# Optimization experiments

Hardware: AMD Instinct MI355X
Metric: run time of the kernel (lower is better)

The kernel has to match this reference:

```python
import jax, jax.numpy as jnp
import numpy as np

B, S, LW = 64, 128, 20
CHAR_V, CHAR_E, CHAR_C = 100, 30, 30
WORD_V, WORD_E = 100000, 300
H, NC = 256, 25
F = WORD_E + CHAR_C  # 330


def setup_inputs() -> dict:
    key = jax.random.key(0)
    ks = jax.random.split(key, 16)
    u = lambda k, shape, s: jax.random.uniform(k, shape, jnp.float32, -s, s)
    sent = jax.random.randint(ks[0], (B, S), 0, WORD_V)
    word = jax.random.randint(ks[1], (B, S, LW), 0, CHAR_V)
    tag = jax.random.randint(ks[2], (B, S), 0, NC)
    lengths = jax.random.randint(ks[3], (B,), S // 2, S + 1)
    mask = jnp.arange(S)[None, :] < lengths[:, None]  # [B,S] bool, mask[:,0] all True

    word_table = u(ks[4], (WORD_V, WORD_E), 0.5)
    char_table = u(ks[5], (CHAR_V, CHAR_E), (3.0 / CHAR_E) ** 0.5)
    conv_w = u(ks[6], (CHAR_C, CHAR_E, 3), (6.0 / (CHAR_E * 3 + CHAR_C)) ** 0.5)
    conv_b = jnp.zeros((CHAR_C,), jnp.float32)

    def lstm_params(k):
        k1, k2 = jax.random.split(k)
        s_ih = (6.0 / (4 * H + F)) ** 0.5
        s_hh = (6.0 / (4 * H + H)) ** 0.5
        w_ih = u(k1, (4 * H, F), s_ih)
        w_hh = u(k2, (4 * H, H), s_hh)
        # b_ih + b_hh, each with forget-gate slice [H:2H] = 1.0 -> combined 2.0
        b = jnp.zeros((4 * H,), jnp.float32).at[H:2 * H].set(2.0)
        return w_ih, w_hh, b

    w_ih_f, w_hh_f, b_f = lstm_params(ks[7])
    w_ih_r, w_hh_r, b_r = lstm_params(ks[8])
    s_lin = (6.0 / (NC + 2 * H)) ** 0.5
    lin_w = u(ks[9], (NC, 2 * H), s_lin)
    lin_b = jnp.zeros((NC,), jnp.float32)
    start_t = u(ks[10], (NC,), 0.1)
    end_t = u(ks[11], (NC,), 0.1)
    trans = u(ks[12], (NC, NC), 0.1)
    return dict(word_table=word_table, char_table=char_table, conv_w=conv_w,
                conv_b=conv_b, w_ih_f=w_ih_f, w_hh_f=w_hh_f, b_f=b_f,
                w_ih_r=w_ih_r, w_hh_r=w_hh_r, b_r=b_r, lin_w=lin_w, lin_b=lin_b,
                start_t=start_t, end_t=end_t, trans=trans,
                sent=sent, word=word, tag=tag, mask=mask)


def _lstm_dir(x, w_ih, w_hh, b, reverse):
    # x: [B,S,F] -> precompute input projections time-major [S,B,4H]
    gx = jnp.einsum('bsf,gf->sbg', x, w_ih) + b
    bsz = x.shape[0]
    hs = w_hh.shape[1]

    def step(carry, g):
        h, c = carry
        g = g + h @ w_hh.T
        i, f, gg, o = jnp.split(g, 4, axis=-1)
        c = jax.nn.sigmoid(f) * c + jax.nn.sigmoid(i) * jnp.tanh(gg)
        h = jax.nn.sigmoid(o) * jnp.tanh(c)
        return (h, c), h

    init = (jnp.zeros((bsz, hs), x.dtype), jnp.zeros((bsz, hs), x.dtype))
    _, hseq = jax.lax.scan(step, init, gx, reverse=reverse)
    return hseq  # [S,B,H]


def _crf_nll(em, tg, mk, start_t, end_t, trans):
    # em: [S,B,C] emissions; tg: [S,B] int; mk: [S,B] float (mk[0]=1)
    bsz = em.shape[1]
    bidx = jnp.arange(bsz)
    # numerator: gold path score
    em_tag = jnp.take_along_axis(em, tg[..., None], axis=-1)[..., 0]   # [S,B]
    tr = trans[tg[:-1], tg[1:]]                                        # [S-1,B]
    score = start_t[tg[0]] + em_tag[0] + jnp.sum(mk[1:] * (tr + em_tag[1:]), axis=0)
    last = mk.sum(0).astype(jnp.int32) - 1
    score = score + end_t[tg[last, bidx]]
    # denominator: forward algorithm (logsumexp scan over time)
    alpha0 = start_t[None, :] + em[0]                                   # [B,C]

    def step(alpha, xs):
        em_t, mk_t = xs
        nxt = jax.nn.logsumexp(alpha[:, :, None] + trans[None, :, :] + em_t[:, None, :], axis=1)
        alpha = jnp.where(mk_t[:, None] > 0, nxt, alpha)
        return alpha, None

    alpha, _ = jax.lax.scan(step, alpha0, (em[1:], mk[1:]))
    logZ = jax.nn.logsumexp(alpha + end_t[None, :], axis=1)
    return -jnp.sum(score - logZ)  # model returns -log_likelihood (reduction='sum')


def reference(word_table, char_table, conv_w, conv_b, w_ih_f, w_hh_f, b_f,
              w_ih_r, w_hh_r, b_r, lin_w, lin_b, start_t, end_t, trans,
              sent, word, tag, mask):
    # --- char CNN encoder (dropout = identity in eval; no ReLU in original forward) ---
    ct = char_table.at[0].set(0.0)                      # padding_idx=0
    cemb = ct[word]                                     # [B,S,LW,E]
    x = cemb.reshape(B * S, LW, CHAR_E).transpose(0, 2, 1)  # [BS,E,LW]
    conv = jax.lax.conv_general_dilated(
        x, conv_w, window_strides=(1,), padding=[(1, 1)],
        dimension_numbers=('NCH', 'OIH', 'NCH')) + conv_b[None, :, None]
    char_feat = conv.max(axis=2).reshape(B, S, CHAR_C)  # global max-pool over chars
    # --- word embedding + concat ---
    wemb = word_table[sent]                             # [B,S,WORD_E]
    feat = jnp.concatenate([wemb, char_feat], axis=2)   # [B,S,F]
    # --- biLSTM ---
    hf = _lstm_dir(feat, w_ih_f, w_hh_f, b_f, reverse=False)
    hr = _lstm_dir(feat, w_ih_r, w_hh_r, b_r, reverse=True)
    h = jnp.concatenate([hf, hr], axis=-1)              # [S,B,2H] time-major
    em = h @ lin_w.T + lin_b                            # [S,B,NC]
    # --- CRF negative log-likelihood ---
    tg = tag.T
    mk = mask.T.astype(em.dtype)
    return _crf_nll(em, tg, mk, start_t, end_t, trans)
```

## Files before the change

### kernel.cpp

```cpp
#include <hip/hip_runtime.h>
#include <math.h>

#define B_  64
#define S_  128
#define LW_ 20
#define CHAR_E_ 30
#define CHAR_C_ 30
#define WORD_E_ 300
#define H_  256
#define NC_ 25
#define F_  330
#define KP_ 352
#define G4_ 1024
#define NG_ 2048

typedef __attribute__((ext_vector_type(8))) short short8;
typedef __attribute__((ext_vector_type(4))) float floatx4;
typedef __attribute__((ext_vector_type(8))) int int8v;

__device__ __forceinline__ float sigmoidf_(float x){ return 1.0f/(1.0f+__expf(-x)); }
__device__ __forceinline__ float tanh_(float x){ return 1.0f - 2.0f/(1.0f+__expf(2.0f*x)); }

__device__ __forceinline__ unsigned int f2bf(float f){
    unsigned int u = __float_as_uint(f);
    u += 0x7FFFu + ((u>>16)&1u);
    return (u>>16) & 0xFFFFu;
}
__device__ __forceinline__ float bf2f(unsigned int v){ return __uint_as_float(v<<16); }

__device__ __forceinline__ void gload16(const void* g, void* l){
    __builtin_amdgcn_global_load_lds((const __attribute__((address_space(1))) unsigned int*)g,
                                     (__attribute__((address_space(3))) unsigned int*)l, 16, 0, 0);
}

#define BAR_LDS() __asm__ volatile("s_waitcnt lgkmcnt(0)\n\ts_barrier" ::: "memory")

__global__ __launch_bounds__(256) void k_prep(const float* ct, const int* word,
        const float* cw, const float* cb, const float* wt, const int* sent,
        const float* wf, const float* wr, float* out,
        unsigned short* feat, unsigned short* wpack){
    __shared__ __align__(16) float x[8][32][20];
    int blk = blockIdx.x;
    int tid = threadIdx.x;
    if(blk < 1024){
        int tok0 = blk*8;
        for(int e = tid; e < 8*32*20; e += 256){
            int t  = e % 20;
            int ic = (e/20) & 31;
            int tl = e / 640;
            int id = word[(size_t)(tok0+tl)*LW_ + t];
            float v = 0.f;
            if(ic < CHAR_E_ && id != 0) v = ct[(size_t)id*CHAR_E_ + ic];
            x[tl][ic][t] = v;
        }
        __syncthreads();
        if(tid < 240){
            int tl = tid/30, oc = tid%30;
            float acc[22];
            #pragma unroll
            for(int q=0;q<22;q++) acc[q] = 0.f;
            for(int ic=0; ic<CHAR_E_; ic++){
                float w0 = cw[(oc*CHAR_E_+ic)*3+0];
                float w1 = cw[(oc*CHAR_E_+ic)*3+1];
                float w2 = cw[(oc*CHAR_E_+ic)*3+2];
                const float* xr = &x[tl][ic][0];
                #pragma unroll
                for(int t4=0;t4<5;t4++){
                    float4 v = ((const float4*)xr)[t4];
                    int t0 = t4*4;
                    acc[t0+2] += v.x*w0; acc[t0+1] += v.x*w1; acc[t0+0] += v.x*w2;
                    acc[t0+3] += v.y*w0; acc[t0+2] += v.y*w1; acc[t0+1] += v.y*w2;
                    acc[t0+4] += v.z*w0; acc[t0+3] += v.z*w1; acc[t0+2] += v.z*w2;
                    acc[t0+5] += v.w*w0; acc[t0+4] += v.w*w1; acc[t0+3] += v.w*w2;
                }
            }
            float m = -1e30f;
            #pragma unroll
            for(int t=0;t<20;t++){ float v = acc[t+1]; m = fmaxf(m, v); }
            m += cb[oc];
            feat[(size_t)(tok0+tl)*KP_ + WORD_E_ + oc] = (unsigned short)f2bf(m);
        }
    } else if(blk < 1024+2432){
        int idx = (blk-1024)*256 + tid;
        int n = idx / 76, e4 = idx % 76;
        if(e4 < 75){
            float4 v = ((const float4*)(wt + (size_t)sent[n]*WORD_E_))[e4];
            unsigned int lo = f2bf(v.x) | (f2bf(v.y)<<16);
            unsigned int hi = f2bf(v.z) | (f2bf(v.w)<<16);
            uint2 pr; pr.x = lo; pr.y = hi;
            *(uint2*)(feat + (size_t)n*KP_ + e4*4) = pr;
        } else {
            unsigned int* z = (unsigned int*)(feat + (size_t)n*KP_ + 330);
            #pragma unroll
            for(int q=0;q<11;q++) z[q] = 0;
        }
    } else if(blk < 6272){
        int i = (blk-3456)*256 + tid;
        int r = i / KP_, k = i % KP_;
        const float* src = (r < G4_) ? wf : wr;
        int rr = r & (G4_-1);
        wpack[i] = (k < F_) ? (unsigned short)f2bf(src[(size_t)rr*F_ + k]) : 0;
    } else {
        if(tid == 0) *out = 0.f;
    }
}

__global__ __launch_bounds__(256) void k_gemm(const unsigned short* A, const unsigned short* Bw,
                                              const float* bf, const float* br, unsigned short* gxb){
    __shared__ __align__(16) unsigned short As[128*32];
    __shared__ __align__(16) unsigned short Bs[128*32];
    int m0 = blockIdx.x*128, n0 = blockIdx.y*128;
    int tid = threadIdx.x;
    int w = tid>>6, lane = tid&63, q = lane>>4, l16 = lane&15;
    int wr = w>>1, wc = w&1;
    int srow0 = w*32 + (lane>>2);
    int scol  = (lane&3)*8;
    floatx4 acc[4][4];
    #pragma unroll
    for(int i=0;i<4;i++)
        #pragma unroll
        for(int j=0;j<4;j++) acc[i][j] = (floatx4){0.f,0.f,0.f,0.f};

    for(int k0=0; k0<KP_; k0+=32){
        __syncthreads();
        gload16(A  + (size_t)(m0+srow0   )*KP_ + k0 + scol, (unsigned short*)As + w*1024      );
        gload16(A  + (size_t)(m0+srow0+16)*KP_ + k0 + scol, (unsigned short*)As + w*1024 + 512);
        gload16(Bw + (size_t)(n0+srow0   )*KP_ + k0 + scol, (unsigned short*)Bs + w*1024      );
        gload16(Bw + (size_t)(n0+srow0+16)*KP_ + k0 + scol, (unsigned short*)Bs + w*1024 + 512);
        __asm__ volatile("s_waitcnt vmcnt(0)" ::: "memory");
        __syncthreads();
        short8 a_[4], b_[4];
        #pragma unroll
        for(int i=0;i<4;i++) a_[i] = *(const short8*)&As[(wr*64 + i*16 + l16)*32 + q*8];
        #pragma unroll
        for(int j=0;j<4;j++) b_[j] = *(const short8*)&Bs[(wc*64 + j*16 + l16)*32 + q*8];
        #pragma unroll
        for(int i=0;i<4;i++)
            #pragma unroll
            for(int j=0;j<4;j++)
                acc[i][j] = __builtin_amdgcn_mfma_f32_16x16x32_bf16(a_[i], b_[j], acc[i][j], 0,0,0);
    }
    #pragma unroll
    for(int j=0;j<4;j++){
        int n = n0 + wc*64 + j*16 + l16;
        int dirr = n >> 10, grow = n & 1023;
        float bias = dirr ? br[grow] : bf[grow];
        #pragma unroll
        for(int i=0;i<4;i++){
            int mb = m0 + wr*64 + i*16 + q*4;
            #pragma unroll
            for(int r=0;r<4;r++){
                gxb[(size_t)(mb+r)*NG_ + n] = (unsigned short)f2bf(acc[i][j][r] + bias);
            }
        }
    }
}

__device__ __forceinline__ void lstm_step(
    const unsigned char* hbb, unsigned char* hwr_slot,
    float* wreg_lds, const int8v (*wreg)[2][2],
    int l16, int q, int cbl, int urel,
    unsigned int G0, unsigned int G1, unsigned int G2, unsigned int G3,
    float& cc, float* hseq_ptr, const float inv_sc)
{
    floatx4 a00={0.f,0.f,0.f,0.f}, a01=a00, a10=a00, a11=a00,
            a20=a00, a21=a00, a30=a00, a31=a00;
    #pragma unroll
    for(int ki=0; ki<2; ki++){
        int8v hb = *(const int8v*)&hbb[l16*272 + ki*128 + q*32];
        a00 = __builtin_amdgcn_mfma_scale_f32_16x16x128_f8f6f4(wreg[0][0][ki], hb, a00, 0,0,0,0x7F,0,0x7F);
        a01 = __builtin_amdgcn_mfma_scale_f32_16x16x128_f8f6f4(wreg[0][1][ki], hb, a01, 0,0,0,0x7F,0,0x7F);
        a10 = __builtin_amdgcn_mfma_scale_f32_16x16x128_f8f6f4(wreg[1][0][ki], hb, a10, 0,0,0,0x7F,0,0x7F);
        a11 = __builtin_amdgcn_mfma_scale_f32_16x16x128_f8f6f4(wreg[1][1][ki], hb, a11, 0,0,0,0x7F,0,0x7F);
        a20 = __builtin_amdgcn_mfma_scale_f32_16x16x128_f8f6f4(wreg[2][0][ki], hb, a20, 0,0,0,0x7F,0,0x7F);
        a21 = __builtin_amdgcn_mfma_scale_f32_16x16x128_f8f6f4(wreg[2][1][ki], hb, a21, 0,0,0,0x7F,0,0x7F);
        a30 = __builtin_amdgcn_mfma_scale_f32_16x16x128_f8f6f4(wreg[3][0][ki], hb, a30, 0,0,0,0x7F,0,0x7F);
        a31 = __builtin_amdgcn_mfma_scale_f32_16x16x128_f8f6f4(wreg[3][1][ki], hb, a31, 0,0,0,0x7F,0,0x7F);
    }
    if(l16 < 2){
        int base = l16*32 + q*4;
        *(floatx4*)&wreg_lds[0*64 + base     ] = a00;
        *(floatx4*)&wreg_lds[0*64 + base + 16] = a01;
        *(floatx4*)&wreg_lds[1*64 + base     ] = a10;
        *(floatx4*)&wreg_lds[1*64 + base + 16] = a11;
        *(floatx4*)&wreg_lds[2*64 + base     ] = a20;
        *(floatx4*)&wreg_lds[2*64 + base + 16] = a21;
        *(floatx4*)&wreg_lds[3*64 + base     ] = a30;
        *(floatx4*)&wreg_lds[3*64 + base + 16] = a31;
    }
    int cidx = cbl*32 + urel;
    float iv = wreg_lds[0*64 + cidx]*inv_sc + bf2f(G0);
    float fv = wreg_lds[1*64 + cidx]*inv_sc + bf2f(G1);
    float gv = wreg_lds[2*64 + cidx]*inv_sc + bf2f(G2);
    float ov = wreg_lds[3*64 + cidx]*inv_sc + bf2f(G3);
    float cn = sigmoidf_(fv)*cc + sigmoidf_(iv)*tanh_(gv);
    cc = cn;
    float hv = sigmoidf_(ov)*tanh_(cn);
    *hseq_ptr = hv;
    unsigned int hp8 = __builtin_amdgcn_cvt_pk_fp8_f32(hv*16.f, hv*16.f, 0u, false);
    *hwr_slot = (unsigned char)(hp8 & 0xFF);
    BAR_LDS();
}

__global__ __launch_bounds__(512,2) void k_lstm_all(const float* whhf, const float* whhr,
        const unsigned short* gxb, float* hseq)
{
    int bid = blockIdx.x;
    int dir = bid >> 5;
    int bg  = bid & 31;
    int tid = threadIdx.x;
    int w    = tid >> 6;
    int lane = tid & 63;
    int q    = lane >> 4;
    int l16  = lane & 15;

    __shared__ __align__(16) unsigned char hlds[2][16*272];
    __shared__ __align__(16) float wregion[8*256];

    const float* whh = dir ? whhr : whhf;

    int8v wreg[4][2][2];
    #pragma unroll
    for(int g=0; g<4; g++){
        #pragma unroll
        for(int j=0; j<2; j++){
            const float* rp = whh + (size_t)(g*H_ + w*32 + j*16 + l16)*H_;
            #pragma unroll
            for(int ki=0; ki<2; ki++){
                const float* p = rp + ki*128 + q*32;
                int8v acc;
                #pragma unroll
                for(int wd=0; wd<8; wd++){
                    unsigned int d = 0;
                    d = __builtin_amdgcn_cvt_pk_fp8_f32(p[wd*4+0]*64.f, p[wd*4+1]*64.f, d, false);
                    d = __builtin_amdgcn_cvt_pk_fp8_f32(p[wd*4+2]*64.f, p[wd*4+3]*64.f, d, true);
                    acc[wd] = (int)d;
                }
                wreg[g][j][ki] = acc;
            }
        }
    }

    for(int i = tid; i < 2*16*272/4; i += 512) ((unsigned int*)hlds)[i] = 0;
    __syncthreads();

    int urel = lane & 31;
    int cbl  = lane >> 5;
    int cu   = w*32 + urel;
    int b_glob = bg*2 + cbl;
    const float inv_sc = 1.0f/1024.f;

    float cc = 0.f;
    const unsigned short* gbase = gxb + (size_t)b_glob*S_*NG_ + (size_t)dir*G4_ + cu;
    float* hseq_base = hseq + ((size_t)dir*S_*B_ + b_glob)*H_ + cu;
    unsigned char* hw0 = &hlds[0][cbl*272 + cu];
    unsigned char* hw1 = &hlds[1][cbl*272 + cu];
    float* wreg_lds = &wregion[w*256];

    unsigned int p0,p1,p2,p3, q0,q1,q2,q3;
    {
        const unsigned short* gp = gbase + (size_t)(dir ? (S_-1) : 0)*NG_;
        p0 = gp[0]; p1 = gp[256]; p2 = gp[512]; p3 = gp[768];
    }

    for(int t=0; t<S_; t+=2){
        int sA = dir ? (S_-1-t) : t;
        int sB = dir ? (S_-2-t) : (t+1);
        int sC = (t+2 < S_) ? (dir ? (S_-3-t) : (t+2)) : sB;

        {
            const unsigned short* gp = gbase + (size_t)sB*NG_;
            q0 = gp[0]; q1 = gp[256]; q2 = gp[512]; q3 = gp[768];
        }
        lstm_step(&hlds[0][0], hw1, wreg_lds, wreg, l16, q, cbl, urel,
                  p0,p1,p2,p3, cc, hseq_base + (size_t)sA*B_*H_, inv_sc);

        {
            const unsigned short* gp = gbase + (size_t)sC*NG_;
            p0 = gp[0]; p1 = gp[256]; p2 = gp[512]; p3 = gp[768];
        }
        lstm_step(&hlds[1][0], hw0, wreg_lds, wreg, l16, q, cbl, urel,
                  q0,q1,q2,q3, cc, hseq_base + (size_t)sB*B_*H_, inv_sc);
    }
}

__global__ __launch_bounds__(256) void k_em(const float* hseq, const float* lw, const float* lb, float* em){
    __shared__ __align__(16) float hb[8][516];
    int sb0 = blockIdx.x*8;
    int tid = threadIdx.x;
    for(int i = tid; i < 1024; i += 256){
        int p = i >> 7, r = i & 127;
        int sb = sb0 + p, s = sb >> 6, b = sb & 63;
        const float* src = (r < 64) ? (hseq + (((size_t)0*S_+s)*B_+b)*H_ + r*4)
                                    : (hseq + (((size_t)1*S_+s)*B_+b)*H_ + (r-64)*4);
        *(float4*)&hb[p][r*4] = *(const float4*)src;
    }
    __syncthreads();
    if(tid < 200){
        int p = tid / 25, nc = tid % 25;
        const float4* wv = (const float4*)(lw + (size_t)nc*2*H_);
        const float4* hv = (const float4*)&hb[p][0];
        float acc = lb[nc];
        #pragma unroll 16
        for(int k=0;k<128;k++){ float4 a=hv[k], ww=wv[k]; acc += a.x*ww.x + a.y*ww.y + a.z*ww.z + a.w*ww.w; }
        em[(size_t)(sb0+p)*NC_ + nc] = acc;
    }
}

__global__ void k_crf(const float* em, const int* tag, const void* mask,
                      const float* st, const float* et, const float* tr, float* out){
    __shared__ float trs[NC_*NC_];
    int b = blockIdx.x, tid = threadIdx.x;
    for(int i=tid;i<NC_*NC_;i+=64) trs[i]=tr[i];
    unsigned int first = *(const unsigned int*)mask;
    int ml;
    if(first == 1u) ml = 0;
    else if(first == 0x3F800000u) ml = 2;
    else ml = 1;
    __syncthreads();

    float part = 0.f; int cnt = 0;
    for(int s = tid; s < S_; s += 64){
        float mkv;
        {
            int off = b*S_ + s;
            if(ml==0)      mkv = ((const int*)mask)[off] ? 1.f : 0.f;
            else if(ml==1) mkv = ((const unsigned char*)mask)[off] ? 1.f : 0.f;
            else           mkv = ((const float*)mask)[off];
        }
        cnt += (mkv != 0.f) ? 1 : 0;
        if(s == 0){
            int t0 = tag[b*S_];
            part += st[t0] + em[((size_t)0*B_ + b)*NC_ + t0];
        } else {
            int tp = tag[b*S_ + s-1], tc = tag[b*S_ + s];
            part += mkv * (trs[tp*NC_ + tc] + em[((size_t)s*B_ + b)*NC_ + tc]);
        }
    }
    for(int o=32;o>0;o>>=1){ part += __shfl_down(part, o); cnt += __shfl_down(cnt, o); }
    float score = 0.f;
    int len = __shfl(cnt, 0);
    float score0 = __shfl(part, 0);
    if(tid == 0) score = score0 + et[ tag[b*S_ + len-1] ];

    float Ecol[NC_];
    if(tid < NC_){
        #pragma unroll
        for(int i=0;i<NC_;i++) Ecol[i] = __expf(trs[i*NC_+tid]);
    } else {
        #pragma unroll
        for(int i=0;i<NC_;i++) Ecol[i] = 0.f;
    }

    float alpha = (tid < NC_) ? (st[tid] + em[((size_t)0*B_ + b)*NC_ + tid]) : -1e30f;
    float em_n = (tid < NC_) ? em[((size_t)1*B_ + b)*NC_ + tid] : 0.f;

    for(int s=1;s<S_;s++){
        float em_c = em_n;
        if(s+1 < S_) em_n = (tid < NC_) ? em[((size_t)(s+1)*B_ + b)*NC_ + tid] : 0.f;
        float mkv;
        {
            int off = b*S_ + s;
            if(ml==0)      mkv = ((const int*)mask)[off] ? 1.f : 0.f;
            else if(ml==1) mkv = ((const unsigned char*)mask)[off] ? 1.f : 0.f;
            else           mkv = ((const float*)mask)[off];
        }
        float v = alpha;
        #pragma unroll
        for(int o=16;o>0;o>>=1) v = fmaxf(v, __shfl_down(v, o));
        float m = __shfl(v, 0);
        float a = (tid < NC_) ? __expf(alpha - m) : 0.f;
        float S0 = 0.f, S1 = 0.f;
        #pragma unroll
        for(int i=0;i<24;i+=2){ S0 += __shfl(a, i) * Ecol[i]; S1 += __shfl(a, i+1) * Ecol[i+1]; }
        S0 += __shfl(a, 24) * Ecol[24];
        float nxt = m + __logf(S0 + S1) + em_c;
        if(tid < NC_ && mkv != 0.f) alpha = nxt;
    }

    float v = (tid < NC_) ? (alpha + et[tid]) : -1e30f;
    float m2 = v;
    #pragma unroll
    for(int o=16;o>0;o>>=1) m2 = fmaxf(m2, __shfl_down(m2, o));
    m2 = __shfl(m2, 0);
    float e = (tid < NC_) ? __expf(v - m2) : 0.f;
    #pragma unroll
    for(int o=16;o>0;o>>=1) e += __shfl_down(e, o);
    if(tid == 0){
        float logZ = m2 + __logf(e);
        atomicAdd(out, logZ - score);
    }
}

extern "C" void kernel_launch(void* const* d_in, const int* in_sizes, int n_in,
                              void* d_out, int out_size, void* d_ws, size_t ws_size,
                              hipStream_t stream) {
    const float* word_table = (const float*)d_in[0];
    const float* char_table = (const float*)d_in[1];
    const float* conv_w     = (const float*)d_in[2];
    const float* conv_b     = (const float*)d_in[3];
    const float* w_ih_f     = (const float*)d_in[4];
    const float* w_hh_f     = (const float*)d_in[5];
    const float* b_f        = (const float*)d_in[6];
    const float* w_ih_r     = (const float*)d_in[7];
    const float* w_hh_r     = (const float*)d_in[8];
    const float* b_r        = (const float*)d_in[9];
    const float* lin_w      = (const float*)d_in[10];
    const float* lin_b      = (const float*)d_in[11];
    const float* start_t    = (const float*)d_in[12];
    const float* end_t      = (const float*)d_in[13];
    const float* trans      = (const float*)d_in[14];
    const int*   sent       = (const int*)d_in[15];
    const int*   word       = (const int*)d_in[16];
    const int*   tag        = (const int*)d_in[17];
    const void*  mask       = d_in[18];
    float* out = (float*)d_out;

    char* ws = (char*)d_ws;
    unsigned short* feat  = (unsigned short*)ws;
    unsigned short* wpack = (unsigned short*)(ws + 5767168);
    unsigned short* gxb   = (unsigned short*)(ws + 5767168 + 1441792);
    float* hseq = (float*)(ws + 5767168 + 1441792 + 33554432);
    float* em   = (float*)(ws + 5767168 + 1441792 + 33554432 + 16777216);

    k_prep<<<dim3(6273), 256, 0, stream>>>(char_table, word, conv_w, conv_b,
                                           word_table, sent, w_ih_f, w_ih_r, out, feat, wpack);
    k_gemm<<<dim3(B_*S_/128, NG_/128), 256, 0, stream>>>(feat, wpack, b_f, b_r, gxb);
    k_lstm_all<<<dim3(64), 512, 0, stream>>>(w_hh_f, w_hh_r, gxb, hseq);
    k_em<<<dim3(S_*B_/8), 256, 0, stream>>>(hseq, lin_w, lin_b, em);
    k_crf<<<dim3(B_), 64, 0, stream>>>(em, tag, mask, start_t, end_t, trans, out);
}
```

Before: 569.2 us.

## Process 16 batch rows per LSTM block using full MFMA output, drop LDS gate exchange

The recurrent LSTM kernel previously used 64 blocks, each handling 2 batch rows, so most of each 16-wide MFMA output was wasted. The gates then went through an LDS round-trip so each thread could pick one unit. Now each block handles 16 batch rows, and each lane applies the cell update directly on its own accumulator registers (8 values per lane). It also writes h and the fp8 copy as vectors and prefetches packed bf16 gate inputs. The grid drops from 64 to 8 blocks. That removes the redundant MFMA work and one LDS exchange plus reads per step, but leaves most CUs idle and puts more elementwise work on each thread.

```diff
diff --git a/kernel.cpp b/kernel.cpp
--- a/kernel.cpp
+++ b/kernel.cpp
@@ -27,6 +27,11 @@
     return (u>>16) & 0xFFFFu;
 }
 __device__ __forceinline__ float bf2f(unsigned int v){ return __uint_as_float(v<<16); }
+
+__device__ __forceinline__ float bfh(uint2 pk, int r){
+    unsigned int w = (r < 2) ? pk.x : pk.y;
+    return __uint_as_float((r & 1) ? (w & 0xffff0000u) : (w << 16));
+}
 
 __device__ __forceinline__ void gload16(const void* g, void* l){
     __builtin_amdgcn_global_load_lds((const __attribute__((address_space(1))) unsigned int*)g,
@@ -156,49 +161,47 @@
     }
 }
 
-__device__ __forceinline__ void lstm_step(
-    const unsigned char* hbb, unsigned char* hwr_slot,
-    float* wreg_lds, const int8v (*wreg)[2][2],
-    int l16, int q, int cbl, int urel,
-    unsigned int G0, unsigned int G1, unsigned int G2, unsigned int G3,
-    float& cc, float* hseq_ptr, const float inv_sc)
+__device__ __forceinline__ void lstm_step16(
+    const unsigned char* hbb, unsigned char* hpub,
+    const int8v (*wreg)[2][2],
+    int l16, int q,
+    const uint2 (&gg)[4][2],
+    float (&cc)[2][4], float* hs_ptr, const float inv_sc)
 {
-    floatx4 a00={0.f,0.f,0.f,0.f}, a01=a00, a10=a00, a11=a00,
-            a20=a00, a21=a00, a30=a00, a31=a00;
+    floatx4 a[4][2];
+    #pragma unroll
+    for(int g=0; g<4; g++){
+        a[g][0] = (floatx4){0.f,0.f,0.f,0.f};
+        a[g][1] = (floatx4){0.f,0.f,0.f,0.f};
+    }
     #pragma unroll
     for(int ki=0; ki<2; ki++){
         int8v hb = *(const int8v*)&hbb[l16*272 + ki*128 + q*32];
-        a00 = __builtin_amdgcn_mfma_scale_f32_16x16x128_f8f6f4(wreg[0][0][ki], hb, a00, 0,0,0,0x7F,0,0x7F);
-        a01 = __builtin_amdgcn_mfma_scale_f32_16x16x128_f8f6f4(wreg[0][1][ki], hb, a01, 0,0,0,0x7F,0,0x7F);
-        a10 = __builtin_amdgcn_mfma_scale_f32_16x16x128_f8f6f4(wreg[1][0][ki], hb, a10, 0,0,0,0x7F,0,0x7F);
-        a11 = __builtin_amdgcn_mfma_scale_f32_16x16x128_f8f6f4(wreg[1][1][ki], hb, a11, 0,0,0,0x7F,0,0x7F);
-        a20 = __builtin_amdgcn_mfma_scale_f32_16x16x128_f8f6f4(wreg[2][0][ki], hb, a20, 0,0,0,0x7F,0,0x7F);
-        a21 = __builtin_amdgcn_mfma_scale_f32_16x16x128_f8f6f4(wreg[2][1][ki], hb, a21, 0,0,0,0x7F,0,0x7F);
-        a30 = __builtin_amdgcn_mfma_scale_f32_16x16x128_f8f6f4(wreg[3][0][ki], hb, a30, 0,0,0,0x7F,0,0x7F);
-        a31 = __builtin_amdgcn_mfma_scale_f32_16x16x128_f8f6f4(wreg[3][1][ki], hb, a31, 0,0,0,0x7F,0,0x7F);
-    }
-    if(l16 < 2){
-        int base = l16*32 + q*4;
-        *(floatx4*)&wreg_lds[0*64 + base     ] = a00;
-        *(floatx4*)&wreg_lds[0*64 + base + 16] = a01;
-        *(floatx4*)&wreg_lds[1*64 + base     ] = a10;
-        *(floatx4*)&wreg_lds[1*64 + base + 16] = a11;
-        *(floatx4*)&wreg_lds[2*64 + base     ] = a20;
-        *(floatx4*)&wreg_lds[2*64 + base + 16] = a21;
-        *(floatx4*)&wreg_lds[3*64 + base     ] = a30;
-        *(floatx4*)&wreg_lds[3*64 + base + 16] = a31;
-    }
-    int cidx = cbl*32 + urel;
-    float iv = wreg_lds[0*64 + cidx]*inv_sc + bf2f(G0);
-    float fv = wreg_lds[1*64 + cidx]*inv_sc + bf2f(G1);
-    float gv = wreg_lds[2*64 + cidx]*inv_sc + bf2f(G2);
-    float ov = wreg_lds[3*64 + cidx]*inv_sc + bf2f(G3);
-    float cn = sigmoidf_(fv)*cc + sigmoidf_(iv)*tanh_(gv);
-    cc = cn;
-    float hv = sigmoidf_(ov)*tanh_(cn);
-    *hseq_ptr = hv;
-    unsigned int hp8 = __builtin_amdgcn_cvt_pk_fp8_f32(hv*16.f, hv*16.f, 0u, false);
-    *hwr_slot = (unsigned char)(hp8 & 0xFF);
+        #pragma unroll
+        for(int g=0; g<4; g++){
+            a[g][0] = __builtin_amdgcn_mfma_scale_f32_16x16x128_f8f6f4(wreg[g][0][ki], hb, a[g][0], 0,0,0,0x7F,0,0x7F);
+            a[g][1] = __builtin_amdgcn_mfma_scale_f32_16x16x128_f8f6f4(wreg[g][1][ki], hb, a[g][1], 0,0,0,0x7F,0,0x7F);
+        }
+    }
+    #pragma unroll
+    for(int j=0; j<2; j++){
+        float hv[4];
+        #pragma unroll
+        for(int r=0; r<4; r++){
+            float iv = a[0][j][r]*inv_sc + bfh(gg[0][j], r);
+            float fv = a[1][j][r]*inv_sc + bfh(gg[1][j], r);
+            float gv = a[2][j][r]*inv_sc + bfh(gg[2][j], r);
+            float ov = a[3][j][r]*inv_sc + bfh(gg[3][j], r);
+            float cn = sigmoidf_(fv)*cc[j][r] + sigmoidf_(iv)*tanh_(gv);
+            cc[j][r] = cn;
+            hv[r] = sigmoidf_(ov)*tanh_(cn);
+        }
+        float4 hv4; hv4.x = hv[0]; hv4.y = hv[1]; hv4.z = hv[2]; hv4.w = hv[3];
+        *(float4*)(hs_ptr + j*16) = hv4;
+        unsigned int d = __builtin_amdgcn_cvt_pk_fp8_f32(hv[0]*16.f, hv[1]*16.f, 0u, false);
+        d = __builtin_amdgcn_cvt_pk_fp8_f32(hv[2]*16.f, hv[3]*16.f, d, true);
+        *(unsigned int*)(hpub + j*16) = d;
+    }
     BAR_LDS();
 }
 
@@ -206,8 +209,8 @@
         const unsigned short* gxb, float* hseq)
 {
     int bid = blockIdx.x;
-    int dir = bid >> 5;
-    int bg  = bid & 31;
+    int dir = bid >> 2;
+    int bg  = bid & 3;
     int tid = threadIdx.x;
     int w    = tid >> 6;
     int lane = tid & 63;
@@ -215,7 +218,6 @@
     int l16  = lane & 15;
 
     __shared__ __align__(16) unsigned char hlds[2][16*272];
-    __shared__ __align__(16) float wregion[8*256];
 
     const float* whh = dir ? whhr : whhf;
 
@@ -244,43 +246,50 @@
     for(int i = tid; i < 2*16*272/4; i += 512) ((unsigned int*)hlds)[i] = 0;
     __syncthreads();
 
-    int urel = lane & 31;
-    int cbl  = lane >> 5;
-    int cu   = w*32 + urel;
-    int b_glob = bg*2 + cbl;
+    int b_glob = bg*16 + l16;
     const float inv_sc = 1.0f/1024.f;
 
-    float cc = 0.f;
-    const unsigned short* gbase = gxb + (size_t)b_glob*S_*NG_ + (size_t)dir*G4_ + cu;
-    float* hseq_base = hseq + ((size_t)dir*S_*B_ + b_glob)*H_ + cu;
-    unsigned char* hw0 = &hlds[0][cbl*272 + cu];
-    unsigned char* hw1 = &hlds[1][cbl*272 + cu];
-    float* wreg_lds = &wregion[w*256];
-
-    unsigned int p0,p1,p2,p3, q0,q1,q2,q3;
-    {
-        const unsigned short* gp = gbase + (size_t)(dir ? (S_-1) : 0)*NG_;
-        p0 = gp[0]; p1 = gp[256]; p2 = gp[512]; p3 = gp[768];
-    }
+    float cc[2][4];
+    #pragma unroll
+    for(int j=0;j<2;j++){
+        #pragma unroll
+        for(int r=0;r<4;r++) cc[j][r]=0.f;
+    }
+
+    long gstep = dir ? -(long)NG_ : (long)NG_;
+    const unsigned short* gp = gxb + ((size_t)b_glob*S_ + (size_t)(dir ? (S_-1) : 0))*NG_
+                               + (size_t)dir*G4_ + w*32 + q*4;
+    long hstep = dir ? -(long)(B_*H_) : (long)(B_*H_);
+    float* hp = hseq + (((size_t)dir*S_ + (size_t)(dir ? (S_-1) : 0))*B_ + b_glob)*H_ + w*32 + q*4;
+
+    unsigned char* hw0 = &hlds[0][l16*272 + w*32 + q*4];
+    unsigned char* hw1 = &hlds[1][l16*272 + w*32 + q*4];
+
+    uint2 P[4][2], Q[4][2];
+    #pragma unroll
+    for(int g=0;g<4;g++){
+        #pragma unroll
+        for(int j=0;j<2;j++) P[g][j] = *(const uint2*)(gp + g*256 + j*16);
+    }
+    gp += gstep;
 
     for(int t=0; t<S_; t+=2){
-        int sA = dir ? (S_-1-t) : t;
-        int sB = dir ? (S_-2-t) : (t+1);
-        int sC = (t+2 < S_) ? (dir ? (S_-3-t) : (t+2)) : sB;
-
-        {
-            const unsigned short* gp = gbase + (size_t)sB*NG_;
-            q0 = gp[0]; q1 = gp[256]; q2 = gp[512]; q3 = gp[768];
-        }
-        lstm_step(&hlds[0][0], hw1, wreg_lds, wreg, l16, q, cbl, urel,
-                  p0,p1,p2,p3, cc, hseq_base + (size_t)sA*B_*H_, inv_sc);
-
-        {
-            const unsigned short* gp = gbase + (size_t)sC*NG_;
-            p0 = gp[0]; p1 = gp[256]; p2 = gp[512]; p3 = gp[768];
-        }
-        lstm_step(&hlds[1][0], hw0, wreg_lds, wreg, l16, q, cbl, urel,
-                  q0,q1,q2,q3, cc, hseq_base + (size_t)sB*B_*H_, inv_sc);
+        #pragma unroll
+        for(int g=0;g<4;g++){
+            #pragma unroll
+            for(int j=0;j<2;j++) Q[g][j] = *(const uint2*)(gp + g*256 + j*16);
+        }
+        gp += gstep;
+        lstm_step16(&hlds[0][0], hw1, wreg, l16, q, P, cc, hp, inv_sc);
+        hp += hstep;
+        #pragma unroll
+        for(int g=0;g<4;g++){
+            #pragma unroll
+            for(int j=0;j<2;j++) P[g][j] = *(const uint2*)(gp + g*256 + j*16);
+        }
+        gp += gstep;
+        lstm_step16(&hlds[1][0], hw0, wreg, l16, q, Q, cc, hp, inv_sc);
+        hp += hstep;
     }
 }
 
@@ -426,7 +435,7 @@
     k_prep<<<dim3(6273), 256, 0, stream>>>(char_table, word, conv_w, conv_b,
                                            word_table, sent, w_ih_f, w_ih_r, out, feat, wpack);
     k_gemm<<<dim3(B_*S_/128, NG_/128), 256, 0, stream>>>(feat, wpack, b_f, b_r, gxb);
-    k_lstm_all<<<dim3(64), 512, 0, stream>>>(w_hh_f, w_hh_r, gxb, hseq);
+    k_lstm_all<<<dim3(8), 512, 0, stream>>>(w_hh_f, w_hh_r, gxb, hseq);
     k_em<<<dim3(S_*B_/8), 256, 0, stream>>>(hseq, lin_w, lin_b, em);
     k_crf<<<dim3(B_), 64, 0, stream>>>(em, tag, mask, start_t, end_t, trans, out);
 }
```

Result: slower. 993.1 us (+74.5%).
